# Kernel tuning notes

Hardware: AMD Instinct MI355X
Metric: run time of the kernel (lower is better)

## Reference

```python
import jax, jax.numpy as jnp
import numpy as np

B, N, D, K = 8, 4096, 128, 1024


def setup_inputs() -> dict:
    key = jax.random.key(0)
    kx, kp = jax.random.split(key)
    x = jax.random.normal(kx, (B, N, D), dtype=jnp.float32)
    # matches nn.Parameter(...).uniform_(-0.1, 0.1)
    prototypes = jax.random.uniform(kp, (K, D), dtype=jnp.float32, minval=-0.1, maxval=0.1)
    return {"x": x, "prototypes": prototypes, "hard": 1}


def reference(x, prototypes, hard):
    x_sq = jnp.sum(x * x, axis=-1, keepdims=True)            # [B,N,1]
    p_sq = jnp.sum(prototypes * prototypes, axis=-1)         # [K]
    xp = jnp.einsum('bnd,kd->bnk', x, prototypes)            # [B,N,K]
    scores = -(x_sq + p_sq[None, None, :] - 2.0 * xp)        # [B,N,K]
    if bool(hard):
        idx = jnp.argmax(scores, axis=-1)                    # [B,N]
        matched = prototypes[idx]                            # [B,N,D]
    else:
        w = jax.nn.softmax(scores, axis=-1)                  # [B,N,K]
        matched = jnp.einsum('bnk,kd->bnd', w, prototypes)   # [B,N,D]
    return (matched, scores)
```

## Files before the change

### kernel.cpp

```cpp
#include <hip/hip_runtime.h>

typedef short short8 __attribute__((ext_vector_type(8)));
typedef float f32x4  __attribute__((ext_vector_type(4)));

constexpr int M_TOT  = 8 * 4096;
constexpr int K_PROT = 1024;
constexpr int D_DIM  = 128;

constexpr size_t WS_PSQ_OFF = (size_t)M_TOT * 4;
constexpr size_t WS_PF_OFF  = WS_PSQ_OFF + (size_t)K_PROT * 4;

__device__ inline unsigned short bf16_hi(float f) {
  unsigned u = __builtin_bit_cast(unsigned, f);
  unsigned r = u + 0x7FFFu + ((u >> 16) & 1u);
  return (unsigned short)(r >> 16);
}
__device__ inline float bf16_tof(unsigned short h) {
  return __builtin_bit_cast(float, (unsigned)h << 16);
}

__device__ inline void barrier_lds() {
  asm volatile("s_waitcnt lgkmcnt(0)\n\ts_barrier" ::: "memory");
}

__global__ __launch_bounds__(256) void norms_kernel(
    const float* __restrict__ x, const float* __restrict__ p,
    float* __restrict__ xsq, float* __restrict__ psq) {
  int group = blockIdx.x * (blockDim.x >> 5) + (threadIdx.x >> 5);
  int lane  = threadIdx.x & 31;
  if (group >= M_TOT + K_PROT) return;
  const float* row = (group < M_TOT) ? (x + (size_t)group * D_DIM)
                                     : (p + (size_t)(group - M_TOT) * D_DIM);
  float4 v = reinterpret_cast<const float4*>(row)[lane];
  float s = v.x * v.x + v.y * v.y + v.z * v.z + v.w * v.w;
  #pragma unroll
  for (int off = 16; off > 0; off >>= 1) s += __shfl_down(s, off, 32);
  if (lane == 0) {
    if (group < M_TOT) xsq[group] = s;
    else psq[group - M_TOT] = s;
  }
}

__global__ __launch_bounds__(256) void pfrag_kernel(
    const float* __restrict__ p, short* __restrict__ pf) {
  int g    = blockIdx.x * 256 + threadIdx.x;
  int lane = g & 63;
  int s    = (g >> 6) & 7;
  int ng   = g >> 9;
  int part = s >> 2, ks = s & 3;
  int proto = ng * 16 + (lane & 15);
  int k0    = ks * 32 + (lane >> 4) * 8;
  const float4* pr = (const float4*)(p + (size_t)proto * D_DIM + k0);
  float4 a = pr[0], b = pr[1];
  float e[8] = {a.x, a.y, a.z, a.w, b.x, b.y, b.z, b.w};
  short8 frag;
  #pragma unroll
  for (int j = 0; j < 8; ++j) {
    unsigned short h = bf16_hi(e[j]);
    if (part) h = bf16_hi(e[j] - bf16_tof(h));
    frag[j] = (short)h;
  }
  *(short8*)(pf + (size_t)g * 8) = frag;
}

__global__ __launch_bounds__(256, 2) void proto_mfma(
    const float* __restrict__ x, const float* __restrict__ p,
    const short* __restrict__ pf, const float* __restrict__ xsq,
    const float* __restrict__ psq,
    float* __restrict__ matched, float* __restrict__ scores) {
  __shared__ short xlds[32 * 64 * 8];
  __shared__ float sbuf[64][132];
  __shared__ float sv[4][64];
  __shared__ int   si[4][64];
  __shared__ int   fidx[64];

  const int tid = threadIdx.x;
  const int w   = tid >> 6;
  const int l   = tid & 63;
  const int m0  = blockIdx.x * 64;

  #pragma unroll
  for (int i = 0; i < 8; ++i) {
    int piece = i * 256 + tid;
    int lane = piece & 63;
    int s = piece >> 6;
    int ks = s & 3, nt = (s >> 2) & 3, part = s >> 4;
    int pix = m0 + nt * 16 + (lane & 15);
    int k0  = ks * 32 + (lane >> 4) * 8;
    const float4* xr = (const float4*)(x + (size_t)pix * D_DIM + k0);
    float4 a = xr[0], b = xr[1];
    float e[8] = {a.x, a.y, a.z, a.w, b.x, b.y, b.z, b.w};
    short8 frag;
    #pragma unroll
    for (int j = 0; j < 8; ++j) {
      unsigned short h = bf16_hi(e[j]);
      if (part) h = bf16_hi(e[j] - bf16_tof(h));
      frag[j] = (short)h;
    }
    *(short8*)(xlds + (size_t)piece * 8) = frag;
  }
  __syncthreads();

  float xs[4];
  #pragma unroll
  for (int nt = 0; nt < 4; ++nt) xs[nt] = xsq[m0 + nt * 16 + (l & 15)];

  float best[4]; int bidx[4];
  #pragma unroll
  for (int nt = 0; nt < 4; ++nt) { best[nt] = -3.4e38f; bidx[nt] = 0; }

  for (int chunk = 0; chunk < 4; ++chunk) {
    f32x4 acc[4][4];
    #pragma unroll
    for (int mt = 0; mt < 4; ++mt)
      #pragma unroll
      for (int nt = 0; nt < 4; ++nt) acc[mt][nt] = (f32x4){0.f, 0.f, 0.f, 0.f};

    const int pgbase = chunk * 16 + w * 4;

    #pragma unroll
    for (int ks = 0; ks < 4; ++ks) {
      short8 pah[4], pal[4], bh[4], bl[4];
      #pragma unroll
      for (int mt = 0; mt < 4; ++mt) {
        pah[mt] = *(const short8*)(pf + ((size_t)((pgbase + mt) * 8 + ks) * 64 + l) * 8);
        pal[mt] = *(const short8*)(pf + ((size_t)((pgbase + mt) * 8 + 4 + ks) * 64 + l) * 8);
      }
      #pragma unroll
      for (int nt = 0; nt < 4; ++nt) {
        bh[nt] = *(const short8*)(xlds + (size_t)(((nt * 4 + ks) * 64) + l) * 8);
        bl[nt] = *(const short8*)(xlds + (size_t)(((16 + nt * 4 + ks) * 64) + l) * 8);
      }
      #pragma unroll
      for (int mt = 0; mt < 4; ++mt)
        #pragma unroll
        for (int nt = 0; nt < 4; ++nt)
          acc[mt][nt] = __builtin_amdgcn_mfma_f32_16x16x32_bf16(pah[mt], bh[nt], acc[mt][nt], 0, 0, 0);
      #pragma unroll
      for (int mt = 0; mt < 4; ++mt)
        #pragma unroll
        for (int nt = 0; nt < 4; ++nt)
          acc[mt][nt] = __builtin_amdgcn_mfma_f32_16x16x32_bf16(pah[mt], bl[nt], acc[mt][nt], 0, 0, 0);
      #pragma unroll
      for (int mt = 0; mt < 4; ++mt)
        #pragma unroll
        for (int nt = 0; nt < 4; ++nt)
          acc[mt][nt] = __builtin_amdgcn_mfma_f32_16x16x32_bf16(pal[mt], bh[nt], acc[mt][nt], 0, 0, 0);
    }

    #pragma unroll
    for (int mt = 0; mt < 4; ++mt) {
      int pbase = chunk * 256 + w * 64 + mt * 16 + (l >> 4) * 4;
      float psa[4];
      *(float4*)psa = *(const float4*)(psq + pbase);
      #pragma unroll
      for (int nt = 0; nt < 4; ++nt) {
        f32x4 o;
        {
          #pragma clang fp contract(off)
          #pragma unroll
          for (int r = 0; r < 4; ++r) {
            float t = (xs[nt] + psa[r]) - 2.0f * acc[mt][nt][r];
            o[r] = -t;
            if (o[r] > best[nt]) { best[nt] = o[r]; bidx[nt] = pbase + r; }
          }
        }
        acc[mt][nt] = o;
      }
    }

    #pragma unroll
    for (int h = 0; h < 2; ++h) {
      if ((w >> 1) == h) {
        const int colbase = (w & 1) * 64 + (l >> 4) * 4;
        #pragma unroll
        for (int mt = 0; mt < 4; ++mt)
          #pragma unroll
          for (int nt = 0; nt < 4; ++nt)
            *(f32x4*)&sbuf[nt * 16 + (l & 15)][colbase + mt * 16] = acc[mt][nt];
      }
      barrier_lds();
      const int gbase = chunk * 256 + h * 128;
      #pragma unroll
      for (int ps = 0; ps < 8; ++ps) {
        int idx = ps * 256 + tid;
        int row = idx >> 5;
        int f4  = idx & 31;
        f32x4 v = *(const f32x4*)&sbuf[row][f4 * 4];
        __builtin_nontemporal_store(v,
            (f32x4*)(scores + (size_t)(m0 + row) * K_PROT + gbase + f4 * 4));
      }
      barrier_lds();
    }
  }

  #pragma unroll
  for (int nt = 0; nt < 4; ++nt) {
    #pragma unroll
    for (int m = 16; m <= 32; m <<= 1) {
      float ov = __shfl_xor(best[nt], m);
      int   oi = __shfl_xor(bidx[nt], m);
      if (ov > best[nt] || (ov == best[nt] && oi < bidx[nt])) {
        best[nt] = ov; bidx[nt] = oi;
      }
    }
  }
  if (l < 16) {
    #pragma unroll
    for (int nt = 0; nt < 4; ++nt) {
      sv[w][nt * 16 + l] = best[nt];
      si[w][nt * 16 + l] = bidx[nt];
    }
  }
  __syncthreads();
  if (tid < 64) {
    float v = sv[0][tid]; int bi = si[0][tid];
    #pragma unroll
    for (int e = 1; e < 4; ++e) {
      float vv = sv[e][tid]; int ii = si[e][tid];
      if (vv > v || (vv == v && ii < bi)) { v = vv; bi = ii; }
    }
    fidx[tid] = bi;
  }
  __syncthreads();

  for (int q = tid; q < 64 * 32; q += 256) {
    int pix = q >> 5, f4 = q & 31;
    float4 v = ((const float4*)(p + (size_t)fidx[pix] * D_DIM))[f4];
    __builtin_nontemporal_store(*(f32x4*)&v,
        (f32x4*)(matched + (size_t)(m0 + pix) * D_DIM) + f4);
  }
}

extern "C" void kernel_launch(void* const* d_in, const int* in_sizes, int n_in,
                              void* d_out, int out_size, void* d_ws, size_t ws_size,
                              hipStream_t stream) {
  const float* x = (const float*)d_in[0];
  const float* p = (const float*)d_in[1];

  float* matched = (float*)d_out;
  float* scores  = (float*)d_out + (size_t)M_TOT * D_DIM;

  float* xsq = (float*)d_ws;
  float* psq = (float*)((char*)d_ws + WS_PSQ_OFF);
  short* pf  = (short*)((char*)d_ws + WS_PF_OFF);

  {
    int rows = M_TOT + K_PROT;
    int blocks = (rows + 7) / 8;
    norms_kernel<<<blocks, 256, 0, stream>>>(x, p, xsq, psq);
  }
  pfrag_kernel<<<128, 256, 0, stream>>>(p, pf);
  proto_mfma<<<M_TOT / 64, 256, 0, stream>>>(x, p, pf, xsq, psq, matched, scores);
}
```

Before: 195.1 us.

## Fuse x-norm computation into main kernel and shrink score staging buffer

```diff
diff --git a/kernel.cpp b/kernel.cpp
--- a/kernel.cpp
+++ b/kernel.cpp
@@ -7,8 +7,7 @@
 constexpr int K_PROT = 1024;
 constexpr int D_DIM  = 128;
 
-constexpr size_t WS_PSQ_OFF = (size_t)M_TOT * 4;
-constexpr size_t WS_PF_OFF  = WS_PSQ_OFF + (size_t)K_PROT * 4;
+constexpr size_t WS_PF_OFF = (size_t)K_PROT * 4;
 
 __device__ inline unsigned short bf16_hi(float f) {
   unsigned u = __builtin_bit_cast(unsigned, f);
@@ -23,22 +22,16 @@
   asm volatile("s_waitcnt lgkmcnt(0)\n\ts_barrier" ::: "memory");
 }
 
-__global__ __launch_bounds__(256) void norms_kernel(
-    const float* __restrict__ x, const float* __restrict__ p,
-    float* __restrict__ xsq, float* __restrict__ psq) {
-  int group = blockIdx.x * (blockDim.x >> 5) + (threadIdx.x >> 5);
+__global__ __launch_bounds__(256) void psq_kernel(
+    const float* __restrict__ p, float* __restrict__ psq) {
+  int group = blockIdx.x * 8 + (threadIdx.x >> 5);
   int lane  = threadIdx.x & 31;
-  if (group >= M_TOT + K_PROT) return;
-  const float* row = (group < M_TOT) ? (x + (size_t)group * D_DIM)
-                                     : (p + (size_t)(group - M_TOT) * D_DIM);
-  float4 v = reinterpret_cast<const float4*>(row)[lane];
+  if (group >= K_PROT) return;
+  float4 v = reinterpret_cast<const float4*>(p + (size_t)group * D_DIM)[lane];
   float s = v.x * v.x + v.y * v.y + v.z * v.z + v.w * v.w;
   #pragma unroll
   for (int off = 16; off > 0; off >>= 1) s += __shfl_down(s, off, 32);
-  if (lane == 0) {
-    if (group < M_TOT) xsq[group] = s;
-    else psq[group - M_TOT] = s;
-  }
+  if (lane == 0) psq[group] = s;
 }
 
 __global__ __launch_bounds__(256) void pfrag_kernel(
@@ -63,33 +56,39 @@
   *(short8*)(pf + (size_t)g * 8) = frag;
 }
 
-__global__ __launch_bounds__(256, 2) void proto_mfma(
+__global__ __launch_bounds__(256, 3) void proto_mfma(
     const float* __restrict__ x, const float* __restrict__ p,
-    const short* __restrict__ pf, const float* __restrict__ xsq,
-    const float* __restrict__ psq,
+    const short* __restrict__ pf, const float* __restrict__ psq,
     float* __restrict__ matched, float* __restrict__ scores) {
   __shared__ short xlds[32 * 64 * 8];
-  __shared__ float sbuf[64][132];
+  __shared__ float sbuf[16][260];
   __shared__ float sv[4][64];
   __shared__ int   si[4][64];
   __shared__ int   fidx[64];
+  __shared__ float xsqv[64];
 
   const int tid = threadIdx.x;
   const int w   = tid >> 6;
   const int l   = tid & 63;
   const int m0  = blockIdx.x * 64;
 
+  float (*xpart)[16] = (float(*)[16])&sbuf[0][0];
+
   #pragma unroll
   for (int i = 0; i < 8; ++i) {
     int piece = i * 256 + tid;
-    int lane = piece & 63;
     int s = piece >> 6;
     int ks = s & 3, nt = (s >> 2) & 3, part = s >> 4;
-    int pix = m0 + nt * 16 + (lane & 15);
-    int k0  = ks * 32 + (lane >> 4) * 8;
+    int pix = m0 + nt * 16 + (l & 15);
+    int k0  = ks * 32 + (l >> 4) * 8;
     const float4* xr = (const float4*)(x + (size_t)pix * D_DIM + k0);
     float4 a = xr[0], b = xr[1];
     float e[8] = {a.x, a.y, a.z, a.w, b.x, b.y, b.z, b.w};
+    if (part == 0) {
+      float ss = e[0]*e[0] + e[1]*e[1] + e[2]*e[2] + e[3]*e[3]
+               + e[4]*e[4] + e[5]*e[5] + e[6]*e[6] + e[7]*e[7];
+      xpart[nt * 16 + (l & 15)][ks * 4 + (l >> 4)] = ss;
+    }
     short8 frag;
     #pragma unroll
     for (int j = 0; j < 8; ++j) {
@@ -101,9 +100,17 @@
   }
   __syncthreads();
 
+  if (tid < 64) {
+    float s = 0.f;
+    #pragma unroll
+    for (int j = 0; j < 16; ++j) s += xpart[tid][j];
+    xsqv[tid] = s;
+  }
+  __syncthreads();
+
   float xs[4];
   #pragma unroll
-  for (int nt = 0; nt < 4; ++nt) xs[nt] = xsq[m0 + nt * 16 + (l & 15)];
+  for (int nt = 0; nt < 4; ++nt) xs[nt] = xsqv[nt * 16 + (l & 15)];
 
   float best[4]; int bidx[4];
   #pragma unroll
@@ -160,8 +167,8 @@
           #pragma clang fp contract(off)
           #pragma unroll
           for (int r = 0; r < 4; ++r) {
-            float t = (xs[nt] + psa[r]) - 2.0f * acc[mt][nt][r];
-            o[r] = -t;
+            float s = xs[nt] + psa[r];
+            o[r] = __builtin_fmaf(2.0f, acc[mt][nt][r], -s);
             if (o[r] > best[nt]) { best[nt] = o[r]; bidx[nt] = pbase + r; }
           }
         }
@@ -170,25 +177,17 @@
     }
 
     #pragma unroll
-    for (int h = 0; h < 2; ++h) {
-      if ((w >> 1) == h) {
-        const int colbase = (w & 1) * 64 + (l >> 4) * 4;
-        #pragma unroll
-        for (int mt = 0; mt < 4; ++mt)
-          #pragma unroll
-          for (int nt = 0; nt < 4; ++nt)
-            *(f32x4*)&sbuf[nt * 16 + (l & 15)][colbase + mt * 16] = acc[mt][nt];
-      }
+    for (int r = 0; r < 4; ++r) {
+      #pragma unroll
+      for (int mt = 0; mt < 4; ++mt)
+        *(f32x4*)&sbuf[l & 15][(w << 6) + mt * 16 + ((l >> 4) << 2)] = acc[mt][r];
       barrier_lds();
-      const int gbase = chunk * 256 + h * 128;
-      #pragma unroll
-      for (int ps = 0; ps < 8; ++ps) {
-        int idx = ps * 256 + tid;
-        int row = idx >> 5;
-        int f4  = idx & 31;
-        f32x4 v = *(const f32x4*)&sbuf[row][f4 * 4];
+      #pragma unroll
+      for (int ps = 0; ps < 4; ++ps) {
+        int row = ps * 4 + w;
+        f32x4 v = *(const f32x4*)&sbuf[row][l << 2];
         __builtin_nontemporal_store(v,
-            (f32x4*)(scores + (size_t)(m0 + row) * K_PROT + gbase + f4 * 4));
+            (f32x4*)(scores + (size_t)(m0 + r * 16 + row) * K_PROT + chunk * 256) + l);
       }
       barrier_lds();
     }
@@ -241,15 +240,10 @@
   float* matched = (float*)d_out;
   float* scores  = (float*)d_out + (size_t)M_TOT * D_DIM;
 
-  float* xsq = (float*)d_ws;
-  float* psq = (float*)((char*)d_ws + WS_PSQ_OFF);
+  float* psq = (float*)d_ws;
   short* pf  = (short*)((char*)d_ws + WS_PF_OFF);
 
-  {
-    int rows = M_TOT + K_PROT;
-    int blocks = (rows + 7) / 8;
-    norms_kernel<<<blocks, 256, 0, stream>>>(x, p, xsq, psq);
-  }
+  psq_kernel<<<K_PROT / 8, 256, 0, stream>>>(p, psq);
   pfrag_kernel<<<128, 256, 0, stream>>>(p, pf);
-  proto_mfma<<<M_TOT / 64, 256, 0, stream>>>(x, p, pf, xsq, psq, matched, scores);
-}
+  proto_mfma<<<M_TOT / 64, 256, 0, stream>>>(x, p, pf, psq, matched, scores);
+}
```

Result: slower. 207.7 us (+6.5%).
